# Kernel tuning notes

Measured on AMD Instinct MI355X. Metric: run time of the kernel, lower is better.

## Reference

```python
import jax, jax.numpy as jnp
import numpy as np

B, N, H, Z, C, IN = 4, 32768, 512, 256, 9, 64
N_TRUNK = 4   # fc_2..fc_5
N_HEADS = 4   # xyz, rgb, scale, opacity (n_layers=1 each)
FACTORS = {'xyz': 1.0, 'rgb': 1.0, 'scale': 1.0, 'opacity': 1.0}


def setup_inputs() -> dict:
    key = jax.random.key(0)
    ks = jax.random.split(key, 20)
    rn = lambda k, s, sc=1.0: jax.random.normal(k, s, jnp.float32) * np.float32(sc)
    wg = 1.0 / np.sqrt(H)       # ModLinear weight_gain / sqrt(in_features)
    sg = 1.0 / np.sqrt(Z)       # style-linear init scale
    inp = {
        'pt_feat': rn(ks[0], (B, N, IN)),
        'onehots': jax.random.uniform(ks[1], (B, N, C), jnp.float32),
        'z': rn(ks[2], (B, Z)),
        'fc1_w': rn(ks[3], (H, IN), 1.0 / np.sqrt(IN)),
        'fc1_b': jnp.zeros((H,), jnp.float32),
        'fcma_w': rn(ks[4], (H, C), 1.0 / np.sqrt(C)),
        # stacked ModLinear params: fc_2..fc_5
        'trunk_weight': rn(ks[5], (N_TRUNK, H, H), wg),
        'trunk_walpha': rn(ks[6], (N_TRUNK, H, Z), sg),
        'trunk_balpha': jnp.ones((N_TRUNK, H), jnp.float32),
        'trunk_wbeta': rn(ks[7], (N_TRUNK, H, Z), sg),
        'trunk_bbeta': jnp.zeros((N_TRUNK, H), jnp.float32),
        # stacked ModLinear params: fc_6_{xyz,rgb,scale,opacity}_0
        'head_weight': rn(ks[8], (N_HEADS, H, H), wg),
        'head_walpha': rn(ks[9], (N_HEADS, H, Z), sg),
        'head_balpha': jnp.ones((N_HEADS, H), jnp.float32),
        'head_wbeta': rn(ks[10], (N_HEADS, H, Z), sg),
        'head_bbeta': jnp.zeros((N_HEADS, H), jnp.float32),
        # output heads
        'out_w_xyz': rn(ks[11], (3, H), 1.0 / np.sqrt(H)),
        'out_b_xyz': jnp.zeros((3,), jnp.float32),
        'out_w_rgb': rn(ks[12], (3, H), 1.0 / np.sqrt(H)),
        'out_b_rgb': jnp.zeros((3,), jnp.float32),
        'out_w_scale': rn(ks[13], (3, H), 1.0 / np.sqrt(H)),
        'out_b_scale': jnp.zeros((3,), jnp.float32),
        'out_w_opacity': rn(ks[14], (1, H), 1.0 / np.sqrt(H)),
        'out_b_opacity': jnp.zeros((1,), jnp.float32),
    }
    return inp


def _act(x):
    # LeakyReLU(0.2)
    return jnp.where(x > 0, x, 0.2 * x)


def _modlin(x, z, W, Wa, ba, Wb, bb):
    """ModLinear with bias=False, mod_bias=True, output_mode=True.
    torch: baddbmm(beta, x, (W*alpha).T) == (x*alpha) @ W.T + beta
    x: [B,N,H], z: [B,Z], W: [H,H], Wa/Wb: [H,Z], ba/bb: [H]."""
    alpha = z @ Wa.T + ba            # [B,H] per-batch input scale
    beta = z @ Wb.T + bb             # [B,H] per-batch output bias
    y = jnp.einsum('bni,oi->bno', x * alpha[:, None, :], W)
    return y + beta[:, None, :]


def reference(pt_feat, onehots, z, fc1_w, fc1_b, fcma_w,
              trunk_weight, trunk_walpha, trunk_balpha, trunk_wbeta, trunk_bbeta,
              head_weight, head_walpha, head_balpha, head_wbeta, head_bbeta,
              out_w_xyz, out_b_xyz, out_w_rgb, out_b_rgb,
              out_w_scale, out_b_scale, out_w_opacity, out_b_opacity):
    f = _act(pt_feat @ fc1_w.T + fc1_b + onehots @ fcma_w.T)  # [B,N,H]
    for i in range(N_TRUNK):
        f = _act(_modlin(f, z, trunk_weight[i], trunk_walpha[i], trunk_balpha[i],
                         trunk_wbeta[i], trunk_bbeta[i]))
    heads = [(out_w_xyz, out_b_xyz), (out_w_rgb, out_b_rgb),
             (out_w_scale, out_b_scale), (out_w_opacity, out_b_opacity)]
    outs = []
    for i, (ow, ob) in enumerate(heads):
        g = _act(_modlin(f, z, head_weight[i], head_walpha[i], head_balpha[i],
                         head_wbeta[i], head_bbeta[i]))
        outs.append(g @ ow.T + ob)
    xyz = (jax.nn.sigmoid(outs[0]) - 0.5) * FACTORS['xyz']
    rgb = outs[1] * FACTORS['rgb']
    scale = jnp.clip(outs[2], 1.0, 1.0)
    opacity = jax.nn.sigmoid(outs[3]) * FACTORS['opacity'] + (1.0 - FACTORS['opacity'])
    # concat dict values in fixed key order (xyz,rgb,scale,opacity) -> [B,N,10]
    return jnp.concatenate([xyz, rgb, scale, opacity], axis=-1)
```

## Files before the change

kernel.cpp:

```cpp
#include <hip/hip_runtime.h>
#include <hip/hip_bf16.h>
#include <cstdint>

#define MTOT 131072
#define MC2  65536
#define MCH  32768
#define HDIM 512

typedef _Float16 f16x8 __attribute__((ext_vector_type(8)));
typedef _Float16 f16x4 __attribute__((ext_vector_type(4)));
typedef unsigned short u16x8 __attribute__((ext_vector_type(8)));
typedef unsigned short u16x4 __attribute__((ext_vector_type(4)));
typedef float    f32x4 __attribute__((ext_vector_type(4)));

__device__ __forceinline__ float bf2f(unsigned short u) {
  return __uint_as_float(((unsigned)u) << 16);
}

__device__ __forceinline__ float ldin(const void* p, long i, int isbf) {
  if (isbf) return bf2f(((const unsigned short*)p)[i]);
  return ((const float*)p)[i];
}

__device__ __forceinline__ void load_lds16(const void* g, void* lds) {
  __builtin_amdgcn_global_load_lds(
      (const __attribute__((address_space(1))) void*)(unsigned long long)(uintptr_t)g,
      (__attribute__((address_space(3))) void*)(unsigned int)(uintptr_t)lds,
      16, 0, 0);
}

__global__ void detect_k(const unsigned* __restrict__ balpha, int* __restrict__ flag) {
  if (threadIdx.x == 0) flag[0] = (balpha[0] == 0x3F803F80u) ? 1 : 0;
}

__global__ __launch_bounds__(256)
void prep_ab(const void* __restrict__ z,
             const void* __restrict__ twa, const void* __restrict__ tba,
             const void* __restrict__ twb, const void* __restrict__ tbb,
             const void* __restrict__ hwa, const void* __restrict__ hba,
             const void* __restrict__ hwb, const void* __restrict__ hbb,
             const int* __restrict__ flag,
             float* __restrict__ alphas, float* __restrict__ betas) {
  const int isbf = flag[0];
  const int bid = blockIdx.x;
  const int og = bid & 7, rest = bid >> 3;
  const int l = rest >> 3, p = (rest >> 2) & 1, b = rest & 3;
  __shared__ float zs[256];
  zs[threadIdx.x] = ldin(z, b * 256 + threadIdx.x, isbf);
  __syncthreads();
  const void *Wsrc, *bsrc;
  long wofs, bofs;
  if (l < 4) {
    Wsrc = (p ? twb : twa); wofs = (long)l * 512 * 256;
    bsrc = (p ? tbb : tba); bofs = l * 512;
  } else {
    const int h = (l == 6) ? 3 : (l - 4);
    Wsrc = (p ? hwb : hwa); wofs = (long)h * 512 * 256;
    bsrc = (p ? hbb : hba); bofs = h * 512;
  }
  const int o = og * 64 + (threadIdx.x >> 2);
  const int kq = threadIdx.x & 3;
  float s = 0.f;
  if (isbf) {
    const unsigned short* wp = (const unsigned short*)Wsrc + wofs + (long)o * 256 + kq * 64;
#pragma unroll
    for (int g = 0; g < 8; g++) {
      u16x8 v = *(const u16x8*)(wp + g * 8);
#pragma unroll
      for (int j = 0; j < 8; j++) s += zs[kq * 64 + g * 8 + j] * bf2f(v[j]);
    }
  } else {
    const float* wp = (const float*)Wsrc + wofs + (long)o * 256 + kq * 64;
#pragma unroll
    for (int g = 0; g < 16; g++) {
      f32x4 v = *(const f32x4*)(wp + g * 4);
#pragma unroll
      for (int j = 0; j < 4; j++) s += zs[kq * 64 + g * 4 + j] * v[j];
    }
  }
  s += __shfl_xor(s, 1, 64);
  s += __shfl_xor(s, 2, 64);
  if (kq == 0) {
    float* dst = (p ? betas : alphas) + (l * 4 + b) * 512;
    dst[o] = s + ldin(bsrc, bofs + o, isbf);
  }
}

__global__ void wmod_k(const void* __restrict__ tw, const void* __restrict__ hw,
                       const int* __restrict__ flag,
                       const float* __restrict__ alphas, _Float16* __restrict__ wmod) {
  const int isbf = flag[0];
  const long t = (long)blockIdx.x * 256 + threadIdx.x;
  const long idx = t * 8;
  const int l   = (int)(idx >> 20);
  const long r0 = idx & ((1 << 20) - 1);
  const int b   = (int)(r0 >> 18);
  const int o   = (int)((r0 >> 9) & 511);
  const int k0  = (int)(r0 & 511);
  const void* wsrc; long ofs;
  if (l < 4) { wsrc = tw; ofs = ((long)l << 18) + (o << 9) + k0; }
  else { const int h = (l == 6) ? 3 : (l - 4); wsrc = hw; ofs = ((long)h << 18) + (o << 9) + k0; }
  const float* al = alphas + (l * 4 + b) * 512 + k0;
  f32x4 a0 = *(const f32x4*)(al);
  f32x4 a1 = *(const f32x4*)(al + 4);
  f16x8 d;
  if (isbf) {
    u16x8 w8 = *(const u16x8*)((const unsigned short*)wsrc + ofs);
#pragma unroll
    for (int j = 0; j < 4; j++) d[j] = (_Float16)(bf2f(w8[j]) * a0[j]);
#pragma unroll
    for (int j = 0; j < 4; j++) d[4 + j] = (_Float16)(bf2f(w8[4 + j]) * a1[j]);
  } else {
    f32x4 w0 = *(const f32x4*)((const float*)wsrc + ofs);
    f32x4 w1 = *(const f32x4*)((const float*)wsrc + ofs + 4);
#pragma unroll
    for (int j = 0; j < 4; j++) d[j] = (_Float16)(w0[j] * a0[j]);
#pragma unroll
    for (int j = 0; j < 4; j++) d[4 + j] = (_Float16)(w1[j] * a1[j]);
  }
  *(f16x8*)(wmod + ((long)(l * 4 + b) << 18) + (o << 9) + k0) = d;
}

__global__ __launch_bounds__(256)
void pack_x(const void* __restrict__ pt, const void* __restrict__ oh,
            long pt_ofs, long oh_ofs, const int* __restrict__ flag,
            _Float16* __restrict__ X) {
  const int isbf = flag[0];
  const int m = blockIdx.x * 8 + (threadIdx.x >> 5);
  const int c5 = threadIdx.x & 31;
  f16x4 d;
  if (c5 < 16) {
    if (isbf) {
      u16x4 v = *(const u16x4*)((const unsigned short*)pt + pt_ofs + (long)m * 64 + c5 * 4);
#pragma unroll
      for (int j = 0; j < 4; j++) d[j] = (_Float16)bf2f(v[j]);
    } else {
      f32x4 v = *(const f32x4*)((const float*)pt + pt_ofs + (long)m * 64 + c5 * 4);
#pragma unroll
      for (int j = 0; j < 4; j++) d[j] = (_Float16)v[j];
    }
  } else {
#pragma unroll
    for (int j = 0; j < 4; j++) {
      const int c = c5 * 4 + j;
      d[j] = (c < 73) ? (_Float16)ldin(oh, oh_ofs + (long)m * 9 + (c - 64), isbf) : (_Float16)0.f;
    }
  }
  *(f16x4*)(X + (long)m * 128 + c5 * 4) = d;
}

__global__ void pack_wc(const void* __restrict__ fc1w, const void* __restrict__ fcmaw,
                        const void* __restrict__ fc1b, const int* __restrict__ flag,
                        _Float16* __restrict__ Wc, float* __restrict__ fb32) {
  const int isbf = flag[0];
  const int o = blockIdx.x, c = threadIdx.x;
  float v = 0.f;
  if (c < 64)      v = ldin(fc1w, o * 64 + c, isbf);
  else if (c < 73) v = ldin(fcmaw, o * 9 + c - 64, isbf);
  Wc[o * 128 + c] = (_Float16)v;
  if (c == 0) fb32[o] = ldin(fc1b, o, isbf);
}

__global__ void conv_small(const void* __restrict__ owx, const void* __restrict__ owr,
                           const void* __restrict__ owo, const void* __restrict__ obx,
                           const void* __restrict__ obr, const void* __restrict__ obo,
                           const int* __restrict__ flag, float* __restrict__ dst) {
  const int t = blockIdx.x * 256 + threadIdx.x;
  if (t >= 3591) return;
  const int isbf = flag[0];
  float v;
  if (t < 1536)      v = ldin(owx, t, isbf);
  else if (t < 3072) v = ldin(owr, t - 1536, isbf);
  else if (t < 3584) v = ldin(owo, t - 3072, isbf);
  else if (t < 3587) v = ldin(obx, t - 3584, isbf);
  else if (t < 3590) v = ldin(obr, t - 3587, isbf);
  else               v = ldin(obo, 0, isbf);
  dst[t] = v;
}

__global__ __launch_bounds__(256)
void gemm_k(const _Float16* __restrict__ A, int lda, int K,
            const _Float16* __restrict__ Wb, int ldb, long wstride,
            const float* __restrict__ biasb, int bstride,
            _Float16* __restrict__ C) {
  __shared__ __align__(16) short As[2 * 128 * 32];
  __shared__ __align__(16) short Bs[2 * 128 * 32];
  const int tid = threadIdx.x;
  const int wave = tid >> 6, lane = tid & 63;
  const int zr = blockIdx.z * MCH;
  const int m0 = blockIdx.x * 128;
  const int n0 = blockIdx.y * 128;
  const _Float16* W = Wb + (long)blockIdx.z * wstride;
  const float* bias = biasb + blockIdx.z * bstride;

  const int l4 = lane >> 2;
  const int sw4 = (lane & 3) ^ (l4 & 3);
  const _Float16* aA = A + (long)(zr + m0 + wave * 32 + l4) * lda + sw4 * 8;
  const _Float16* aB = W + (long)(n0 + wave * 32 + l4) * ldb + sw4 * 8;
  short* dA0 = &As[(wave * 32) * 32];
  short* dA1 = &As[(wave * 32 + 16) * 32];
  short* dB0 = &Bs[(wave * 32) * 32];
  short* dB1 = &Bs[(wave * 32 + 16) * 32];

  const int wm = wave >> 1, wn = wave & 1;
  const int fr = lane & 15, fq = lane >> 4;
  const int sq = (fq ^ (fr & 3)) * 8;

  f32x4 acc[4][4] = {};

  load_lds16(aA, dA0);
  load_lds16(aA + 16 * (long)lda, dA1);
  load_lds16(aB, dB0);
  load_lds16(aB + 16 * (long)ldb, dB1);

  const int nIter = K >> 5;
  for (int k = 0; k < nIter; k++) {
    const int cur = (k & 1) << 12;
    __syncthreads();
    if (k + 1 < nIter) {
      const int nxt = ((k + 1) & 1) << 12;
      const long ko = (long)(k + 1) * 32;
      load_lds16(aA + ko, dA0 + nxt);
      load_lds16(aA + ko + 16 * (long)lda, dA1 + nxt);
      load_lds16(aB + ko, dB0 + nxt);
      load_lds16(aB + ko + 16 * (long)ldb, dB1 + nxt);
    }
    f16x8 af[4], bfv[4];
#pragma unroll
    for (int i = 0; i < 4; i++)
      af[i] = *(const f16x8*)&As[cur + (wm * 64 + i * 16 + fr) * 32 + sq];
#pragma unroll
    for (int j = 0; j < 4; j++)
      bfv[j] = *(const f16x8*)&Bs[cur + (wn * 64 + j * 16 + fr) * 32 + sq];
#pragma unroll
    for (int i = 0; i < 4; i++)
#pragma unroll
      for (int j = 0; j < 4; j++)
        acc[i][j] = __builtin_amdgcn_mfma_f32_16x16x32_f16(af[i], bfv[j], acc[i][j], 0, 0, 0);
  }

#pragma unroll
  for (int j = 0; j < 4; j++) {
    const int col = n0 + wn * 64 + j * 16 + fr;
    const float bv = bias[col];
#pragma unroll
    for (int i = 0; i < 4; i++) {
      const long row = (long)zr + m0 + wm * 64 + i * 16 + fq * 4;
#pragma unroll
      for (int r = 0; r < 4; r++) {
        float v = acc[i][j][r] + bv;
        v = v > 0.f ? v : 0.2f * v;
        C[(row + r) * HDIM + col] = (_Float16)v;
      }
    }
  }
}

#define BAR() asm volatile("s_barrier" ::: "memory")
#define VMC(n) asm volatile("s_waitcnt vmcnt(" #n ")" ::: "memory")
#define LGK0() do { asm volatile("s_waitcnt lgkmcnt(0)" ::: "memory"); \
                    __builtin_amdgcn_sched_barrier(0); } while (0)
#define PR1 __builtin_amdgcn_s_setprio(1)
#define PR0 __builtin_amdgcn_s_setprio(0)

__global__ __launch_bounds__(512, 2)
void gemm256_k(const _Float16* __restrict__ A,
               const _Float16* __restrict__ Wb, long wstride,
               const float* __restrict__ biasb, int bstride,
               _Float16* __restrict__ C) {
  __shared__ __align__(16) short As[2][16384];
  __shared__ __align__(16) short Bs[2][16384];
  const int tid = threadIdx.x;
  const int wave = tid >> 6, lane = tid & 63;
  const int gsw = (blockIdx.x & 7) * 64 + (blockIdx.x >> 3);
  const int z = gsw >> 8;
  const int n0 = (gsw & 1) * 256;
  const int m0 = ((gsw >> 1) & 127) * 256;
  const long zr = (long)z * MCH;
  const _Float16* W = Wb + (long)z * wstride;
  const float* bias = biasb + z * bstride;

  const int srow = lane >> 3;
  const int schk = (lane & 7) ^ srow;
  const _Float16* gA = A + (zr + m0 + wave * 8 + srow) * 512L + schk * 8;
  const _Float16* gB = W + ((long)(n0 + wave * 8 + srow)) * 512L + schk * 8;
  short* lA = &As[0][0] + wave * 512;
  short* lB = &Bs[0][0] + wave * 512;

#define STGA(buf, t, j) load_lds16(gA + (t) * 64 + (j) * (64 * 512L), lA + (buf) * 16384 + (j) * 4096)
#define STGB(buf, t, j) load_lds16(gB + (t) * 64 + (j) * (64 * 512L), lB + (buf) * 16384 + (j) * 4096)

  const int fr = lane & 15, fq = lane >> 4;
  const int wm = wave >> 2, wn = wave & 3;
  const int c0 = (fq ^ (fr & 7)) * 8;
  const int c1 = c0 ^ 32;
  const int aB0 = (wm * 128 + fr) * 64;
  const int bB0 = (wn * 64 + fr) * 64;

  f16x8 aLo[4][2], aHi[4][2], bLo[2][2], bHi[2][2];
  f32x4 acc[8][4] = {};

#define RDAL(buf, i) { aLo[i][0] = *(const f16x8*)&As[buf][aB0 + (i) * 1024 + c0]; \
                       aLo[i][1] = *(const f16x8*)&As[buf][aB0 + (i) * 1024 + c1]; }
#define RDAH(buf, i) { aHi[i][0] = *(const f16x8*)&As[buf][aB0 + ((i) + 4) * 1024 + c0]; \
                       aHi[i][1] = *(const f16x8*)&As[buf][aB0 + ((i) + 4) * 1024 + c1]; }
#define RDBL(buf, j) { bLo[j][0] = *(const f16x8*)&Bs[buf][bB0 + (j) * 1024 + c0]; \
                       bLo[j][1] = *(const f16x8*)&Bs[buf][bB0 + (j) * 1024 + c1]; }
#define RDBH(buf, j) { bHi[j][0] = *(const f16x8*)&Bs[buf][bB0 + ((j) + 2) * 1024 + c0]; \
                       bHi[j][1] = *(const f16x8*)&Bs[buf][bB0 + ((j) + 2) * 1024 + c1]; }
#define MMQ(AF, io, BF, jo) { \
  _Pragma("unroll") for (int il = 0; il < 4; il++) \
  _Pragma("unroll") for (int jl = 0; jl < 2; jl++) { \
    acc[(io) + il][(jo) + jl] = __builtin_amdgcn_mfma_f32_16x16x32_f16( \
        AF[il][0], BF[jl][0], acc[(io) + il][(jo) + jl], 0, 0, 0); \
    acc[(io) + il][(jo) + jl] = __builtin_amdgcn_mfma_f32_16x16x32_f16( \
        AF[il][1], BF[jl][1], acc[(io) + il][(jo) + jl], 0, 0, 0); } }

  STGB(0, 0, 0); STGB(0, 0, 1); STGB(0, 0, 2); STGB(0, 0, 3);
  STGA(0, 0, 0); STGA(0, 0, 1); STGA(0, 0, 2); STGA(0, 0, 3);
  STGB(1, 1, 0); STGB(1, 1, 1); STGB(1, 1, 2); STGB(1, 1, 3);
  STGA(1, 1, 0); STGA(1, 1, 1); STGA(1, 1, 2); STGA(1, 1, 3);
  VMC(8); BAR();

#pragma unroll
  for (int t = 0; t < 8; t++) {
    const int buf = t & 1;
    RDAL(buf, 0) RDAL(buf, 1) RDAL(buf, 2) RDAL(buf, 3)
    RDBL(buf, 0) RDBL(buf, 1)
    RDBH(buf, 0) RDBH(buf, 1)
    RDAH(buf, 0) RDAH(buf, 1) RDAH(buf, 2) RDAH(buf, 3)
    PR1; MMQ(aLo, 0, bLo, 0); MMQ(aLo, 0, bHi, 2); PR0;
    LGK0();
    BAR();
    if (t + 2 < 8) { STGB(buf, t + 2, 0); STGB(buf, t + 2, 1);
                     STGB(buf, t + 2, 2); STGB(buf, t + 2, 3);
                     STGA(buf, t + 2, 0); STGA(buf, t + 2, 1);
                     STGA(buf, t + 2, 2); STGA(buf, t + 2, 3); }
    PR1; MMQ(aHi, 4, bLo, 0); MMQ(aHi, 4, bHi, 2); PR0;
    if (t < 6) { VMC(8); } else if (t == 6) { VMC(0); }
    BAR();
  }

  float bv[4];
#pragma unroll
  for (int j = 0; j < 4; j++) bv[j] = bias[n0 + wn * 64 + j * 16 + fr];
#pragma unroll
  for (int i = 0; i < 8; i++) {
    const long row = zr + m0 + wm * 128 + i * 16 + fq * 4;
#pragma unroll
    for (int r = 0; r < 4; r++) {
      _Float16* cp = C + (row + r) * HDIM + n0 + wn * 64 + fr;
#pragma unroll
      for (int j = 0; j < 4; j++) {
        float v = acc[i][j][r] + bv[j];
        v = v > 0.f ? v : 0.2f * v;
        cp[j * 16] = (_Float16)v;
      }
    }
  }
#undef STGA
#undef STGB
#undef RDAL
#undef RDAH
#undef RDBL
#undef RDBH
#undef MMQ
}

template <int MODE>
__global__ __launch_bounds__(256)
void proj_k(const _Float16* __restrict__ g, const float* __restrict__ P,
            const float* __restrict__ ob, const int* __restrict__ flag,
            void* __restrict__ outv, long row0) {
  const int tid = threadIdx.x;
  const int wave = tid >> 6, lane = tid & 63;
  const int rg = lane >> 4, lg = lane & 15;
  const long row = (long)blockIdx.x * 16 + wave * 4 + rg;
  const _Float16* gr = g + row * HDIM;
  float s0 = 0.f, s1 = 0.f, s2 = 0.f;
#pragma unroll
  for (int p = 0; p < 4; p++) {
    const int c0 = p * 128 + lg * 8;
    f16x8 v = *(const f16x8*)(gr + c0);
#pragma unroll
    for (int j = 0; j < 8; j++) {
      float gv = (float)v[j];
      s0 += gv * P[c0 + j];
      if (MODE != 2) {
        s1 += gv * P[512 + c0 + j];
        s2 += gv * P[1024 + c0 + j];
      }
    }
  }
#pragma unroll
  for (int off = 1; off < 16; off <<= 1) {
    s0 += __shfl_xor(s0, off, 64);
    if (MODE != 2) {
      s1 += __shfl_xor(s1, off, 64);
      s2 += __shfl_xor(s2, off, 64);
    }
  }
  if (lg == 0) {
    const long ro = (row0 + row) * 10;
    float v[4]; int c0, nc;
    if (MODE == 0) {
      v[0] = 1.f / (1.f + __expf(-(s0 + ob[0]))) - 0.5f;
      v[1] = 1.f / (1.f + __expf(-(s1 + ob[1]))) - 0.5f;
      v[2] = 1.f / (1.f + __expf(-(s2 + ob[2]))) - 0.5f;
      c0 = 0; nc = 3;
    } else if (MODE == 1) {
      v[0] = s0 + ob[0]; v[1] = s1 + ob[1]; v[2] = s2 + ob[2];
      c0 = 3; nc = 3;
    } else {
      v[0] = 1.0f; v[1] = 1.0f; v[2] = 1.0f;
      v[3] = 1.f / (1.f + __expf(-(s0 + ob[0])));
      c0 = 6; nc = 4;
    }
    if (flag[0]) {
      __hip_bfloat16* o = (__hip_bfloat16*)outv + ro + c0;
      for (int c = 0; c < nc; c++) o[c] = __float2bfloat16(v[c]);
    } else {
      float* o = (float*)outv + ro + c0;
      for (int c = 0; c < nc; c++) o[c] = v[c];
    }
  }
}

extern "C" void kernel_launch(void* const* d_in, const int* in_sizes, int n_in,
                              void* d_out, int out_size, void* d_ws, size_t ws_size,
                              hipStream_t stream) {
  const void* pt    = d_in[0];
  const void* oh    = d_in[1];
  const void* z     = d_in[2];
  const void* fc1w  = d_in[3];
  const void* fc1b  = d_in[4];
  const void* fcmaw = d_in[5];
  const void* tw    = d_in[6];
  const void* twa   = d_in[7];
  const void* tba   = d_in[8];
  const void* twb   = d_in[9];
  const void* tbb   = d_in[10];
  const void* hw    = d_in[11];
  const void* hwa   = d_in[12];
  const void* hba   = d_in[13];
  const void* hwb   = d_in[14];
  const void* hbb   = d_in[15];
  const void* owx   = d_in[16];
  const void* obx   = d_in[17];
  const void* owr   = d_in[18];
  const void* obr   = d_in[19];
  const void* owo   = d_in[22];
  const void* obo   = d_in[23];

  char* ws = (char*)d_ws;
  _Float16* g0    = (_Float16*)(ws + 0);
  _Float16* g1    = (_Float16*)(ws + 67108864LL);
  _Float16* X     = (_Float16*)(ws + 67108864LL);
  _Float16* wmodp = (_Float16*)(ws + 134217728LL);
  _Float16* Wc    = (_Float16*)(ws + 148897792LL);
  float* alphas   = (float*)(ws + 149028864LL);
  float* betas    = (float*)(ws + 149086208LL);
  float* fb32     = (float*)(ws + 149143552LL);
  int*   dflag    = (int*)  (ws + 149145600LL);
  float* ow32     = (float*)(ws + 149145664LL);

  detect_k<<<1, 64, 0, stream>>>((const unsigned*)tba, dflag);
  prep_ab<<<448, 256, 0, stream>>>(z, twa, tba, twb, tbb, hwa, hba, hwb, hbb, dflag, alphas, betas);
  wmod_k<<<3584, 256, 0, stream>>>(tw, hw, dflag, alphas, wmodp);
  pack_wc<<<512, 128, 0, stream>>>(fc1w, fcmaw, fc1b, dflag, Wc, fb32);
  conv_small<<<15, 256, 0, stream>>>(owx, owr, owo, obx, obr, obo, dflag, ow32);

  dim3 gg(MCH / 128, 4, 2), gb(256);
  const int pgrid = MC2 / 16;
  for (int p = 0; p < 2; p++) {
    const long prow = (long)p * MC2;
    pack_x<<<MC2 / 8, 256, 0, stream>>>(pt, oh, prow * 64, prow * 9, dflag, X);
    gemm_k<<<gg, gb, 0, stream>>>(X, 128, 128, Wc, 128, 0, fb32, 0, g0);
    _Float16* fin = g0; _Float16* fout = g1;
    for (int l = 0; l < 4; l++) {
      gemm256_k<<<512, 512, 0, stream>>>(fin, wmodp + (long)(l * 4 + p * 2) * 262144, 262144,
                                         betas + (l * 4 + p * 2) * 512, 512, fout);
      _Float16* t = fin; fin = fout; fout = t;
    }
    gemm256_k<<<512, 512, 0, stream>>>(fin, wmodp + (long)(4 * 4 + p * 2) * 262144, 262144,
                                       betas + (4 * 4 + p * 2) * 512, 512, g1);
    proj_k<0><<<pgrid, 256, 0, stream>>>(g1, ow32, ow32 + 3584, dflag, d_out, prow);
    gemm256_k<<<512, 512, 0, stream>>>(fin, wmodp + (long)(5 * 4 + p * 2) * 262144, 262144,
                                       betas + (5 * 4 + p * 2) * 512, 512, g1);
    proj_k<1><<<pgrid, 256, 0, stream>>>(g1, ow32 + 1536, ow32 + 3587, dflag, d_out, prow);
    gemm256_k<<<512, 512, 0, stream>>>(fin, wmodp + (long)(6 * 4 + p * 2) * 262144, 262144,
                                       betas + (6 * 4 + p * 2) * 512, 512, g1);
    proj_k<2><<<pgrid, 256, 0, stream>>>(g1, ow32 + 3072, ow32 + 3590, dflag, d_out, prow);
  }
}
```

Measured before the change: 888.8 us.

## Fuse output-head projections into head GEMM epilogues with partial-sum buffer

The head GEMMs no longer write their full fp16 activation tensor for a separate projection kernel to read back. Each GEMM epilogue applies bias and LeakyReLU, then dots the tile with the small output-weight rows and reduces across lanes with shuffles. It writes per-slot partial sums to a workspace buffer, and a small finalize kernel sums the 8 slots per output and applies the sigmoid and other output transforms. This removes three large activation writes and reads per half-batch but adds shuffle reductions and scattered partial-sum stores to the GEMM epilogue.

```diff
diff --git a/kernel.cpp b/kernel.cpp
--- a/kernel.cpp
+++ b/kernel.cpp
@@ -263,11 +263,14 @@
 #define PR1 __builtin_amdgcn_s_setprio(1)
 #define PR0 __builtin_amdgcn_s_setprio(0)
 
+template <int NOUT, int CBASE>
 __global__ __launch_bounds__(512, 2)
-void gemm256_k(const _Float16* __restrict__ A,
+void gemm256_t(const _Float16* __restrict__ A,
                const _Float16* __restrict__ Wb, long wstride,
                const float* __restrict__ biasb, int bstride,
-               _Float16* __restrict__ C) {
+               _Float16* __restrict__ C,
+               const float* __restrict__ P,
+               float* __restrict__ part) {
   __shared__ __align__(16) short As[2][16384];
   __shared__ __align__(16) short Bs[2][16384];
   const int tid = threadIdx.x;
@@ -344,17 +347,45 @@
   float bv[4];
 #pragma unroll
   for (int j = 0; j < 4; j++) bv[j] = bias[n0 + wn * 64 + j * 16 + fr];
-#pragma unroll
-  for (int i = 0; i < 8; i++) {
-    const long row = zr + m0 + wm * 128 + i * 16 + fq * 4;
-#pragma unroll
-    for (int r = 0; r < 4; r++) {
-      _Float16* cp = C + (row + r) * HDIM + n0 + wn * 64 + fr;
-#pragma unroll
-      for (int j = 0; j < 4; j++) {
-        float v = acc[i][j][r] + bv[j];
-        v = v > 0.f ? v : 0.2f * v;
-        cp[j * 16] = (_Float16)v;
+
+  if constexpr (NOUT == 0) {
+#pragma unroll
+    for (int i = 0; i < 8; i++) {
+      const long row = zr + m0 + wm * 128 + i * 16 + fq * 4;
+#pragma unroll
+      for (int r = 0; r < 4; r++) {
+        _Float16* cp = C + (row + r) * HDIM + n0 + wn * 64 + fr;
+#pragma unroll
+        for (int j = 0; j < 4; j++) {
+          float v = acc[i][j][r] + bv[j];
+          v = v > 0.f ? v : 0.2f * v;
+          cp[j * 16] = (_Float16)v;
+        }
+      }
+    }
+  } else {
+    const int slot = ((n0 >> 8) << 2) + wn;
+#pragma unroll
+    for (int i = 0; i < 8; i++) {
+#pragma unroll
+      for (int r = 0; r < 4; r++) {
+        const long row = zr + m0 + wm * 128 + i * 16 + fq * 4 + r;
+        float av[4];
+#pragma unroll
+        for (int j = 0; j < 4; j++) {
+          float v = acc[i][j][r] + bv[j];
+          av[j] = v > 0.f ? v : 0.2f * v;
+        }
+#pragma unroll
+        for (int c = 0; c < NOUT; c++) {
+          const float* Pc = P + c * 512 + n0 + wn * 64 + fr;
+          float s = av[0] * Pc[0] + av[1] * Pc[16] + av[2] * Pc[32] + av[3] * Pc[48];
+          s += __shfl_xor(s, 1, 64);
+          s += __shfl_xor(s, 2, 64);
+          s += __shfl_xor(s, 4, 64);
+          s += __shfl_xor(s, 8, 64);
+          if (fr == 0) part[row * 64 + (CBASE + c) * 8 + slot] = s;
+        }
       }
     }
   }
@@ -367,62 +398,34 @@
 #undef MMQ
 }
 
-template <int MODE>
 __global__ __launch_bounds__(256)
-void proj_k(const _Float16* __restrict__ g, const float* __restrict__ P,
-            const float* __restrict__ ob, const int* __restrict__ flag,
-            void* __restrict__ outv, long row0) {
-  const int tid = threadIdx.x;
-  const int wave = tid >> 6, lane = tid & 63;
-  const int rg = lane >> 4, lg = lane & 15;
-  const long row = (long)blockIdx.x * 16 + wave * 4 + rg;
-  const _Float16* gr = g + row * HDIM;
-  float s0 = 0.f, s1 = 0.f, s2 = 0.f;
-#pragma unroll
-  for (int p = 0; p < 4; p++) {
-    const int c0 = p * 128 + lg * 8;
-    f16x8 v = *(const f16x8*)(gr + c0);
-#pragma unroll
-    for (int j = 0; j < 8; j++) {
-      float gv = (float)v[j];
-      s0 += gv * P[c0 + j];
-      if (MODE != 2) {
-        s1 += gv * P[512 + c0 + j];
-        s2 += gv * P[1024 + c0 + j];
-      }
-    }
-  }
-#pragma unroll
-  for (int off = 1; off < 16; off <<= 1) {
-    s0 += __shfl_xor(s0, off, 64);
-    if (MODE != 2) {
-      s1 += __shfl_xor(s1, off, 64);
-      s2 += __shfl_xor(s2, off, 64);
-    }
-  }
-  if (lg == 0) {
-    const long ro = (row0 + row) * 10;
-    float v[4]; int c0, nc;
-    if (MODE == 0) {
-      v[0] = 1.f / (1.f + __expf(-(s0 + ob[0]))) - 0.5f;
-      v[1] = 1.f / (1.f + __expf(-(s1 + ob[1]))) - 0.5f;
-      v[2] = 1.f / (1.f + __expf(-(s2 + ob[2]))) - 0.5f;
-      c0 = 0; nc = 3;
-    } else if (MODE == 1) {
-      v[0] = s0 + ob[0]; v[1] = s1 + ob[1]; v[2] = s2 + ob[2];
-      c0 = 3; nc = 3;
-    } else {
-      v[0] = 1.0f; v[1] = 1.0f; v[2] = 1.0f;
-      v[3] = 1.f / (1.f + __expf(-(s0 + ob[0])));
-      c0 = 6; nc = 4;
-    }
-    if (flag[0]) {
-      __hip_bfloat16* o = (__hip_bfloat16*)outv + ro + c0;
-      for (int c = 0; c < nc; c++) o[c] = __float2bfloat16(v[c]);
-    } else {
-      float* o = (float*)outv + ro + c0;
-      for (int c = 0; c < nc; c++) o[c] = v[c];
-    }
+void fin_k(const float* __restrict__ part, const float* __restrict__ ob,
+           const int* __restrict__ flag, void* __restrict__ outv, long row0) {
+  const long row = (long)blockIdx.x * 256 + threadIdx.x;
+  const float* pr = part + row * 64;
+  float s[7];
+#pragma unroll
+  for (int c = 0; c < 7; c++) {
+    f32x4 a = *(const f32x4*)(pr + c * 8);
+    f32x4 b = *(const f32x4*)(pr + c * 8 + 4);
+    s[c] = ((a[0] + a[1]) + (a[2] + a[3])) + ((b[0] + b[1]) + (b[2] + b[3]));
+  }
+  float v[10];
+#pragma unroll
+  for (int c = 0; c < 3; c++) v[c] = 1.f / (1.f + __expf(-(s[c] + ob[c]))) - 0.5f;
+#pragma unroll
+  for (int c = 0; c < 3; c++) v[3 + c] = s[3 + c] + ob[3 + c];
+  v[6] = 1.0f; v[7] = 1.0f; v[8] = 1.0f;
+  v[9] = 1.f / (1.f + __expf(-(s[6] + ob[6])));
+  const long ro = (row0 + row) * 10;
+  if (flag[0]) {
+    __hip_bfloat16* o = (__hip_bfloat16*)outv + ro;
+#pragma unroll
+    for (int c = 0; c < 10; c++) o[c] = __float2bfloat16(v[c]);
+  } else {
+    float* o = (float*)outv + ro;
+#pragma unroll
+    for (int c = 0; c < 10; c++) o[c] = v[c];
   }
 }
 
@@ -463,6 +466,7 @@
   float* fb32     = (float*)(ws + 149143552LL);
   int*   dflag    = (int*)  (ws + 149145600LL);
   float* ow32     = (float*)(ws + 149145664LL);
+  float* part     = (float*)(ws + 167772160LL);
 
   detect_k<<<1, 64, 0, stream>>>((const unsigned*)tba, dflag);
   prep_ab<<<448, 256, 0, stream>>>(z, twa, tba, twb, tbb, hwa, hba, hwb, hbb, dflag, alphas, betas);
@@ -471,25 +475,26 @@
   conv_small<<<15, 256, 0, stream>>>(owx, owr, owo, obx, obr, obo, dflag, ow32);
 
   dim3 gg(MCH / 128, 4, 2), gb(256);
-  const int pgrid = MC2 / 16;
   for (int p = 0; p < 2; p++) {
     const long prow = (long)p * MC2;
     pack_x<<<MC2 / 8, 256, 0, stream>>>(pt, oh, prow * 64, prow * 9, dflag, X);
     gemm_k<<<gg, gb, 0, stream>>>(X, 128, 128, Wc, 128, 0, fb32, 0, g0);
     _Float16* fin = g0; _Float16* fout = g1;
     for (int l = 0; l < 4; l++) {
-      gemm256_k<<<512, 512, 0, stream>>>(fin, wmodp + (long)(l * 4 + p * 2) * 262144, 262144,
-                                         betas + (l * 4 + p * 2) * 512, 512, fout);
+      gemm256_t<0, 0><<<512, 512, 0, stream>>>(fin, wmodp + (long)(l * 4 + p * 2) * 262144, 262144,
+                                               betas + (l * 4 + p * 2) * 512, 512, fout,
+                                               nullptr, nullptr);
       _Float16* t = fin; fin = fout; fout = t;
     }
-    gemm256_k<<<512, 512, 0, stream>>>(fin, wmodp + (long)(4 * 4 + p * 2) * 262144, 262144,
-                                       betas + (4 * 4 + p * 2) * 512, 512, g1);
-    proj_k<0><<<pgrid, 256, 0, stream>>>(g1, ow32, ow32 + 3584, dflag, d_out, prow);
-    gemm256_k<<<512, 512, 0, stream>>>(fin, wmodp + (long)(5 * 4 + p * 2) * 262144, 262144,
-                                       betas + (5 * 4 + p * 2) * 512, 512, g1);
-    proj_k<1><<<pgrid, 256, 0, stream>>>(g1, ow32 + 1536, ow32 + 3587, dflag, d_out, prow);
-    gemm256_k<<<512, 512, 0, stream>>>(fin, wmodp + (long)(6 * 4 + p * 2) * 262144, 262144,
-                                       betas + (6 * 4 + p * 2) * 512, 512, g1);
-    proj_k<2><<<pgrid, 256, 0, stream>>>(g1, ow32 + 3072, ow32 + 3590, dflag, d_out, prow);
-  }
-}
+    gemm256_t<3, 0><<<512, 512, 0, stream>>>(fin, wmodp + (long)(4 * 4 + p * 2) * 262144, 262144,
+                                             betas + (4 * 4 + p * 2) * 512, 512, nullptr,
+                                             ow32, part);
+    gemm256_t<3, 3><<<512, 512, 0, stream>>>(fin, wmodp + (long)(5 * 4 + p * 2) * 262144, 262144,
+                                             betas + (5 * 4 + p * 2) * 512, 512, nullptr,
+                                             ow32 + 1536, part);
+    gemm256_t<1, 6><<<512, 512, 0, stream>>>(fin, wmodp + (long)(6 * 4 + p * 2) * 262144, 262144,
+                                             betas + (6 * 4 + p * 2) * 512, 512, nullptr,
+                                             ow32 + 3072, part);
+    fin_k<<<MC2 / 256, 256, 0, stream>>>(part, ow32 + 3584, dflag, d_out, prow);
+  }
+}
```

After: 849.8 us. 4.4% less time.
